# Kernel tuning notes

Measured on AMD Instinct MI355X. Metric: run time of the kernel, lower is better.

## Reference

```python
import jax, jax.numpy as jnp
import numpy as np

B = 4; C = 3; IMG = 256; P = 16; HP = 16; HW = 256
DIM = 512; DEPTH = 6; HEADS = 8; DH = 64
NS = 50; SH = 4; SDH = 64; ITERS = 3; RPD = 128; FF = 2048; N = NS + HW


def _ln(x, g, b):
    m = jnp.mean(x, -1, keepdims=True)
    v = jnp.var(x, -1, keepdims=True)
    return (x - m) * jax.lax.rsqrt(v + 1e-5) * g + b


def _rms(x, g):
    # lucidrains RMSNorm: F.normalize(x, dim=-1) * sqrt(dim) * gamma
    n = jnp.linalg.norm(x, axis=-1, keepdims=True)
    return x / jnp.maximum(n, 1e-12) * (DIM ** 0.5) * g


def setup_inputs() -> dict:
    key = jax.random.key(0)
    ks = iter(jax.random.split(key, 64))
    def W(*s):
        return jax.random.normal(next(ks), s, jnp.float32) * 0.02
    SI = SH * SDH
    d = {}
    d['images'] = jax.random.normal(next(ks), (B, C, IMG, IMG), jnp.float32)
    d['slot_noise'] = jax.random.normal(next(ks), (B, NS, DIM), jnp.float32)
    d['patch_w'] = W(C * P * P, DIM); d['patch_b'] = jnp.zeros((DIM,))
    d['hpos'] = W(HP, DIM); d['wpos'] = W(HP, DIM)
    d['rp_w1'] = W(2, RPD); d['rp_b1'] = jnp.zeros((RPD,))
    d['rp_w2'] = W(RPD, RPD); d['rp_b2'] = jnp.zeros((RPD,))
    d['rp_w3'] = W(RPD, HEADS); d['rp_b3'] = jnp.zeros((HEADS,))
    d['slots_mu'] = W(1, 1, DIM); d['slots_logsigma'] = jnp.zeros((1, 1, DIM))
    d['sa_ln_in_g'] = jnp.ones((DIM,)); d['sa_ln_in_b'] = jnp.zeros((DIM,))
    d['sa_ln_sl_g'] = jnp.ones((DIM,)); d['sa_ln_sl_b'] = jnp.zeros((DIM,))
    d['sa_wq'] = W(DIM, SI); d['sa_bq'] = jnp.zeros((SI,))
    d['sa_wk'] = W(DIM, SI); d['sa_bk'] = jnp.zeros((SI,))
    d['sa_wv'] = W(DIM, SI); d['sa_bv'] = jnp.zeros((SI,))
    d['sa_wo'] = W(SI, DIM); d['sa_bo'] = jnp.zeros((DIM,))
    d['gru_wih'] = W(DIM, 3 * DIM); d['gru_whh'] = W(DIM, 3 * DIM)
    d['gru_bih'] = jnp.zeros((3 * DIM,)); d['gru_bhh'] = jnp.zeros((3 * DIM,))
    d['sa_ln_ff_g'] = jnp.ones((DIM,)); d['sa_ln_ff_b'] = jnp.zeros((DIM,))
    d['sa_mlp_w1'] = W(DIM, DIM); d['sa_mlp_b1'] = jnp.zeros((DIM,))
    d['sa_mlp_w2'] = W(DIM, DIM); d['sa_mlp_b2'] = jnp.zeros((DIM,))
    d['s2c_w'] = W(DIM, 2); d['s2c_b'] = jnp.zeros((2,))
    d['attn_g'] = jnp.ones((DEPTH, DIM))
    d['wq'] = W(DEPTH, DIM, HEADS * DH); d['wk'] = W(DEPTH, DIM, HEADS * DH)
    d['wv'] = W(DEPTH, DIM, HEADS * DH); d['wo'] = W(DEPTH, HEADS * DH, DIM)
    d['ff_g'] = jnp.ones((DEPTH, DIM))
    d['ff_w1'] = W(DEPTH, DIM, FF); d['ff_b1'] = jnp.zeros((DEPTH, FF))
    d['ff_w2'] = W(DEPTH, FF, DIM); d['ff_b2'] = jnp.zeros((DEPTH, DIM))
    d['final_g'] = jnp.ones((DIM,))
    d['pred_w'] = W(DIM, DIM); d['pred_b'] = jnp.zeros((DIM,))
    return d


def reference(images, slot_noise, patch_w, patch_b, hpos, wpos,
              rp_w1, rp_b1, rp_w2, rp_b2, rp_w3, rp_b3,
              slots_mu, slots_logsigma, sa_ln_in_g, sa_ln_in_b, sa_ln_sl_g, sa_ln_sl_b,
              sa_wq, sa_bq, sa_wk, sa_bk, sa_wv, sa_bv, sa_wo, sa_bo,
              gru_wih, gru_whh, gru_bih, gru_bhh, sa_ln_ff_g, sa_ln_ff_b,
              sa_mlp_w1, sa_mlp_b1, sa_mlp_w2, sa_mlp_b2, s2c_w, s2c_b,
              attn_g, wq, wk, wv, wo, ff_g, ff_w1, ff_b1, ff_w2, ff_b2,
              final_g, pred_w, pred_b):
    b = images.shape[0]
    # patchify: b c (h p1) (w p2) -> b h w (p1 p2 c)
    x = images.reshape(b, C, HP, P, HP, P).transpose(0, 2, 4, 3, 5, 1).reshape(b, HP, HP, P * P * C)
    tokens = x @ patch_w + patch_b                     # [b, HP, HP, DIM]
    tokens = tokens + hpos[:, None, :] + wpos[None, :, :]
    tokens = tokens.reshape(b, HW, DIM)
    # --- multi-head slot attention ---
    inp = _ln(tokens, sa_ln_in_g, sa_ln_in_b)
    k = (inp @ sa_wk + sa_bk).reshape(b, HW, SH, SDH).transpose(0, 2, 1, 3)
    v = (inp @ sa_wv + sa_bv).reshape(b, HW, SH, SDH).transpose(0, 2, 1, 3)
    slots = slots_mu + jnp.exp(slots_logsigma) * slot_noise  # [b, NS, DIM]
    scale = SDH ** -0.5
    for _ in range(ITERS):
        prev = slots
        s = _ln(slots, sa_ln_sl_g, sa_ln_sl_b)
        q = (s @ sa_wq + sa_bq).reshape(b, NS, SH, SDH).transpose(0, 2, 1, 3)
        dots = jnp.einsum('bhid,bhjd->bhij', q, k) * scale     # [b, SH, NS, HW]
        attn = jax.nn.softmax(dots, axis=-2) + 1e-8            # softmax over slots
        attn = attn / jnp.sum(attn, -1, keepdims=True)         # weighted mean over inputs
        upd = jnp.einsum('bhij,bhjd->bhid', attn, v)
        upd = upd.transpose(0, 2, 1, 3).reshape(b, NS, SH * SDH) @ sa_wo + sa_bo
        # GRUCell(updates, prev_slots)
        gx = upd @ gru_wih + gru_bih
        gh = prev @ gru_whh + gru_bhh
        xr, xz, xn = jnp.split(gx, 3, -1)
        hr, hz, hn = jnp.split(gh, 3, -1)
        r = jax.nn.sigmoid(xr + hr)
        z = jax.nn.sigmoid(xz + hz)
        nn_ = jnp.tanh(xn + r * hn)
        slots = (1 - z) * nn_ + z * prev
        slots = slots + (jax.nn.relu(_ln(slots, sa_ln_ff_g, sa_ln_ff_b) @ sa_mlp_w1 + sa_mlp_b1) @ sa_mlp_w2 + sa_mlp_b2)
    objects = slots
    slot_coords = objects @ s2c_w + s2c_b              # [b, NS, 2]
    # --- relative position MLP bias (slots coords + patch grid) ---
    g = jnp.arange(HP, dtype=jnp.float32)
    grid = jnp.stack(jnp.meshgrid(g, g, indexing='ij'), -1).reshape(HW, 2)
    coords = jnp.concatenate([slot_coords, jnp.broadcast_to(grid, (b, HW, 2))], axis=1)  # [b, N, 2]
    rel = coords[:, :, None, :] - coords[:, None, :, :]   # [b, N, N, 2]
    hmid = jax.nn.silu(rel @ rp_w1 + rp_b1)
    hmid = jax.nn.silu(hmid @ rp_w2 + rp_b2)
    bias = jnp.transpose(hmid @ rp_w3 + rp_b3, (0, 3, 1, 2))  # [b, HEADS, N, N]
    # --- transformer with per-layer rel-pos bias ---
    x = jnp.concatenate([objects, tokens], axis=1)     # [b, N, DIM]
    ascale = DH ** -0.5
    for l in range(DEPTH):
        h = _rms(x, attn_g[l])
        qh = (h @ wq[l]).reshape(b, N, HEADS, DH).transpose(0, 2, 1, 3)
        kh = (h @ wk[l]).reshape(b, N, HEADS, DH).transpose(0, 2, 1, 3)
        vh = (h @ wv[l]).reshape(b, N, HEADS, DH).transpose(0, 2, 1, 3)
        sim = jnp.einsum('bhid,bhjd->bhij', qh, kh) * ascale + bias
        a = jax.nn.softmax(sim, -1)
        o = jnp.einsum('bhij,bhjd->bhid', a, vh).transpose(0, 2, 1, 3).reshape(b, N, HEADS * DH) @ wo[l]
        x = x + o
        h = _rms(x, ff_g[l])
        x = x + (jax.nn.gelu(h @ ff_w1[l] + ff_b1[l]) @ ff_w2[l] + ff_b2[l])
    x = _rms(x, final_g)
    return x[:, NS:] @ pred_w + pred_b                 # [b, HW, DIM]
```

## Files before the change

kernel.cpp:

```cpp
#include <hip/hip_runtime.h>
#include <hip/hip_bf16.h>

typedef __hip_bfloat16 bf16;
typedef short short8v __attribute__((ext_vector_type(8)));
typedef float float4v __attribute__((ext_vector_type(4)));

static __device__ __forceinline__ float b2f(bf16 x){ return __bfloat162float(x); }

static __device__ __forceinline__ float ldin(const void* p, size_t i, bool isbf) {
  return isbf ? b2f(((const bf16*)p)[i]) : ((const float*)p)[i];
}

static __device__ __forceinline__ unsigned short f2bu(float f) {
  bf16 h = __float2bfloat16(f);
  return *reinterpret_cast<unsigned short*>(&h);
}

#define CDIV(a,b) (((a)+(b)-1)/(b))

#define NB   4
#define NSL  50
#define HWT  256
#define NT   306
#define DIM  512
#define NH   8
#define FF   2048
#define RPP  28100
#define PCH  56200

static __device__ __forceinline__ void rp_decode(int q, int& i, int& j) {
  if (q < 15300) { i = q / NT; j = q % NT; }
  else { int r = q - 15300; i = NSL + r / NSL; j = r % NSL; }
}

__global__ void detect_k(const void* p, int* flag) {
  const unsigned short* u = (const unsigned short*)p;
  int t = threadIdx.x;
  int e = (u[t] >> 7) & 0xFF;
  __shared__ int anybad;
  if (t == 0) anybad = 0;
  __syncthreads();
  if (e >= 0x88) atomicOr(&anybad, 1);
  __syncthreads();
  if (t == 0) *flag = anybad ? 0 : 1;
}

__global__ __launch_bounds__(256) void wtrans_k(const void* __restrict__ W,
    unsigned short* __restrict__ WT, int K, int N, const int* __restrict__ flagp) {
  const bool isbf = *flagp != 0;
  __shared__ unsigned short S[64 * 72];
  const size_t slice = (size_t)K * N * blockIdx.z;
  int n0 = blockIdx.x * 64, k0 = blockIdx.y * 64;
  int t = threadIdx.x;
  int kk = t >> 4, nn = (t & 15) * 4;
#pragma unroll
  for (int r = 0; r < 4; ++r) {
    int k = k0 + kk + r * 16;
    unsigned short v[4];
    if (isbf) {
      ushort4 u = *(const ushort4*)((const unsigned short*)W + slice + (size_t)k * N + n0 + nn);
      v[0]=u.x; v[1]=u.y; v[2]=u.z; v[3]=u.w;
    } else {
      float4 f = *(const float4*)((const float*)W + slice + (size_t)k * N + n0 + nn);
      v[0]=f2bu(f.x); v[1]=f2bu(f.y); v[2]=f2bu(f.z); v[3]=f2bu(f.w);
    }
#pragma unroll
    for (int i = 0; i < 4; ++i) S[(nn + i) * 72 + kk + r * 16] = v[i];
  }
  __syncthreads();
  int nr = t >> 2, kc = (t & 3) * 16;
  short8v s0 = *(const short8v*)&S[nr * 72 + kc];
  short8v s1 = *(const short8v*)&S[nr * 72 + kc + 8];
  unsigned short* dst = WT + slice + (size_t)(n0 + nr) * K + k0 + kc;
  *(short8v*)dst = s0;
  *(short8v*)(dst + 8) = s1;
}

#define LDT 40
static __device__ __forceinline__ void gemm_body2(
    const void* __restrict__ A, int aty,
    const unsigned short* __restrict__ WT,
    const void* __restrict__ bias, size_t boff,
    void* __restrict__ C, int oty,
    int M, int N, int K, int kbeg, int kend,
    int act, int mode, bool isbf)
{
  __shared__ unsigned short As[64 * LDT];
  __shared__ unsigned short Bs[64 * LDT];
  const int tid = threadIdx.x;
  const int lane = tid & 63, wave = tid >> 6;
  const int quad = lane >> 4, ti = lane & 15;
  const int wm = (wave & 1) * 32, wn = (wave >> 1) * 32;
  const int bm = blockIdx.y * 64, bn = blockIdx.x * 64;
  const int srow = tid >> 2, sch = (tid & 3) * 8;

  unsigned short ha[8], hb[8];
  const int gm = bm + srow;
  const bool aok = gm < M;
  const unsigned short* Abf = (const unsigned short*)A + (size_t)gm * K;
  const float*          Af  = (const float*)A + (size_t)gm * K;
  const unsigned short* Bp  = WT + (size_t)(bn + srow) * K;

  auto fetchA = [&](int k0) {
    if (aok) {
      if (aty) {
        const ushort4* ap = (const ushort4*)(Abf + k0 + sch);
        ushort4 u0 = ap[0], u1 = ap[1];
        ha[0]=u0.x; ha[1]=u0.y; ha[2]=u0.z; ha[3]=u0.w;
        ha[4]=u1.x; ha[5]=u1.y; ha[6]=u1.z; ha[7]=u1.w;
      } else {
        const float* ap = Af + k0 + sch;
        float4 x = *(const float4*)ap, y = *(const float4*)(ap + 4);
        ha[0]=f2bu(x.x); ha[1]=f2bu(x.y); ha[2]=f2bu(x.z); ha[3]=f2bu(x.w);
        ha[4]=f2bu(y.x); ha[5]=f2bu(y.y); ha[6]=f2bu(y.z); ha[7]=f2bu(y.w);
      }
    } else {
      for (int i = 0; i < 8; ++i) ha[i] = 0;
    }
  };
  auto fetchB = [&](int k0) {
    const ushort4* bp = (const ushort4*)(Bp + k0 + sch);
    ushort4 u0 = bp[0], u1 = bp[1];
    hb[0]=u0.x; hb[1]=u0.y; hb[2]=u0.z; hb[3]=u0.w;
    hb[4]=u1.x; hb[5]=u1.y; hb[6]=u1.z; hb[7]=u1.w;
  };

  float4v acc00 = {0,0,0,0}, acc01 = {0,0,0,0}, acc10 = {0,0,0,0}, acc11 = {0,0,0,0};
  fetchA(kbeg); fetchB(kbeg);
  for (int k0 = kbeg; k0 < kend; k0 += 32) {
    *(short8v*)&As[srow * LDT + sch] = *(short8v*)ha;
    *(short8v*)&Bs[srow * LDT + sch] = *(short8v*)hb;
    __syncthreads();
    if (k0 + 32 < kend) { fetchA(k0 + 32); fetchB(k0 + 32); }
    short8v a0 = *reinterpret_cast<const short8v*>(&As[(wm + ti)      * LDT + quad * 8]);
    short8v a1 = *reinterpret_cast<const short8v*>(&As[(wm + 16 + ti) * LDT + quad * 8]);
    short8v b0 = *reinterpret_cast<const short8v*>(&Bs[(wn + ti)      * LDT + quad * 8]);
    short8v b1 = *reinterpret_cast<const short8v*>(&Bs[(wn + 16 + ti) * LDT + quad * 8]);
    acc00 = __builtin_amdgcn_mfma_f32_16x16x32_bf16(a0, b0, acc00, 0, 0, 0);
    acc01 = __builtin_amdgcn_mfma_f32_16x16x32_bf16(a0, b1, acc01, 0, 0, 0);
    acc10 = __builtin_amdgcn_mfma_f32_16x16x32_bf16(a1, b0, acc10, 0, 0, 0);
    acc11 = __builtin_amdgcn_mfma_f32_16x16x32_bf16(a1, b1, acc11, 0, 0, 0);
    __syncthreads();
  }

  float4v accs[2][2] = {{acc00, acc01}, {acc10, acc11}};
#pragma unroll
  for (int mi = 0; mi < 2; ++mi) {
#pragma unroll
    for (int ni = 0; ni < 2; ++ni) {
      int row0 = bm + wm + mi * 16 + quad * 4;
      int col  = bn + wn + ni * 16 + ti;
      float bv = (bias && kbeg == 0) ? ldin(bias, boff + col, isbf) : 0.f;
#pragma unroll
      for (int r = 0; r < 4; ++r) {
        int row = row0 + r;
        if (row >= M) continue;
        float v = accs[mi][ni][r] + bv;
        if (act == 1) v = fmaxf(v, 0.f);
        else if (act == 2) {
          float u = 0.7978845608028654f * (v + 0.044715f * v * v * v);
          v = 0.5f * v * (1.f + tanhf(u));
        } else if (act == 3) {
          v = v / (1.f + expf(-v));
        }
        size_t idx = (size_t)row * N + col;
        if (oty) ((bf16*)C)[idx] = __float2bfloat16(v);
        else {
          float* Cf = (float*)C;
          if (mode == 2) atomicAdd(&Cf[idx], v);
          else if (mode == 1) Cf[idx] += v;
          else Cf[idx] = v;
        }
      }
    }
  }
}

__global__ __launch_bounds__(256) void gemm_mfma(
    const void* A, int aty, const unsigned short* WT, size_t woff,
    const void* bias, size_t boff, void* C, int oty,
    int M, int N, int K, int act, int accum, int zsplit, const int* __restrict__ flagp)
{
  int ksz = K / zsplit;
  int kbeg = blockIdx.z * ksz;
  int mode = zsplit > 1 ? 2 : (accum ? 1 : 0);
  gemm_body2(A, aty, WT + woff, bias, boff, C, oty, M, N, K, kbeg, kbeg + ksz,
             act, mode, *flagp != 0);
}

__global__ __launch_bounds__(256) void gemm_mfma_tri(
    const void* A, int aty, const unsigned short* WT, size_t o0, size_t o1, size_t o2,
    void* C0, void* C1, void* C2, int oty, int M, int N, int K,
    const int* __restrict__ flagp)
{
  size_t o = blockIdx.z == 0 ? o0 : (blockIdx.z == 1 ? o1 : o2);
  void* C = blockIdx.z == 0 ? C0 : (blockIdx.z == 1 ? C1 : C2);
  gemm_body2(A, aty, WT + o, nullptr, 0, C, oty, M, N, K, 0, K, 0, 0, *flagp != 0);
}

__global__ __launch_bounds__(256) void gemm_mfma_duo(
    const void* A0, const void* A1, int aty, const unsigned short* WT, size_t o0, size_t o1,
    const void* bias0, const void* bias1, void* C0, void* C1, int oty,
    int M, int N, int K, const int* __restrict__ flagp)
{
  const void* A = blockIdx.z ? A1 : A0;
  size_t o = blockIdx.z ? o1 : o0;
  const void* bias = blockIdx.z ? bias1 : bias0;
  void* C = blockIdx.z ? C1 : C0;
  gemm_body2(A, aty, WT + o, bias, 0, C, oty, M, N, K, 0, K, 0, 0, *flagp != 0);
}

__global__ void s2c_k(const float* __restrict__ slots, const void* __restrict__ w,
                      const void* __restrict__ bv, float* __restrict__ sc,
                      const int* __restrict__ flagp) {
  const bool isbf = *flagp != 0;
  int row = blockIdx.x, t = threadIdx.x;
  const float* x = slots + (size_t)row * DIM;
  float v0 = x[t], v1 = x[t + 256];
  float a0 = v0 * ldin(w, 2 * t, isbf)     + v1 * ldin(w, 2 * (t + 256), isbf);
  float a1 = v0 * ldin(w, 2 * t + 1, isbf) + v1 * ldin(w, 2 * (t + 256) + 1, isbf);
  __shared__ float r0[256], r1[256];
  r0[t] = a0; r1[t] = a1;
  __syncthreads();
  for (int o = 128; o > 0; o >>= 1) {
    if (t < o) { r0[t] += r0[t + o]; r1[t] += r1[t + o]; }
    __syncthreads();
  }
  if (t == 0) {
    sc[row * 2]     = r0[0] + ldin(bv, 0, isbf);
    sc[row * 2 + 1] = r1[0] + ldin(bv, 1, isbf);
  }
}

__global__ void patchify_k(const void* __restrict__ img, unsigned short* __restrict__ xp,
                           const int* __restrict__ flagp) {
  const bool isbf = *flagp != 0;
  int i = blockIdx.x * 256 + threadIdx.x;
  if (i >= NB * HWT * 768) return;
  int col = i % 768, row = i / 768;
  int c = col % 3, p2 = (col / 3) & 15, p1 = col / 48;
  int w = row & 15, h = (row >> 4) & 15, b = row >> 8;
  xp[i] = f2bu(ldin(img, (((size_t)(b * 3 + c) * 256 + h * 16 + p1) * 256) + w * 16 + p2, isbf));
}

__global__ void addpos_k(float* __restrict__ tok, const void* __restrict__ hp,
                         const void* __restrict__ wp, const int* __restrict__ flagp) {
  const bool isbf = *flagp != 0;
  int i = blockIdx.x * 256 + threadIdx.x;
  if (i >= NB * HWT * DIM) return;
  int d = i & 511;
  int row = i >> 9;
  int w = row & 15, h = (row >> 4) & 15;
  tok[i] += ldin(hp, h * DIM + d, isbf) + ldin(wp, w * DIM + d, isbf);
}

__global__ void ln512_k(const float* __restrict__ X, const void* __restrict__ g,
                        const void* __restrict__ b, unsigned short* __restrict__ Y,
                        const int* __restrict__ flagp) {
  const bool isbf = *flagp != 0;
  int row = blockIdx.x, t = threadIdx.x;
  const float* x = X + (size_t)row * DIM;
  float v0 = x[t], v1 = x[t + 256];
  __shared__ float rs[256], rq[256];
  rs[t] = v0 + v1; rq[t] = v0 * v0 + v1 * v1;
  __syncthreads();
  for (int o = 128; o > 0; o >>= 1) {
    if (t < o) { rs[t] += rs[t + o]; rq[t] += rq[t + o]; }
    __syncthreads();
  }
  float mean = rs[0] * (1.f / 512.f);
  float var  = rq[0] * (1.f / 512.f) - mean * mean;
  float inv  = rsqrtf(var + 1e-5f);
  unsigned short* y = Y + (size_t)row * DIM;
  y[t]       = f2bu((v0 - mean) * inv * ldin(g, t, isbf)       + ldin(b, t, isbf));
  y[t + 256] = f2bu((v1 - mean) * inv * ldin(g, t + 256, isbf) + ldin(b, t + 256, isbf));
}

__global__ void rms512_k(const float* __restrict__ X, const void* __restrict__ g,
                         int goff, unsigned short* __restrict__ Y, const int* __restrict__ flagp) {
  const bool isbf = *flagp != 0;
  int row = blockIdx.x, t = threadIdx.x;
  const float* x = X + (size_t)row * DIM;
  float v0 = x[t], v1 = x[t + 256];
  __shared__ float rq[256];
  rq[t] = v0 * v0 + v1 * v1;
  __syncthreads();
  for (int o = 128; o > 0; o >>= 1) {
    if (t < o) rq[t] += rq[t + o];
    __syncthreads();
  }
  float nrm = sqrtf(rq[0]);
  float sc = 22.62741699796952f / fmaxf(nrm, 1e-12f);
  unsigned short* y = Y + (size_t)row * DIM;
  y[t]       = f2bu(v0 * sc * ldin(g, goff + t, isbf));
  y[t + 256] = f2bu(v1 * sc * ldin(g, goff + t + 256, isbf));
}

__global__ void slots_init_k(const void* __restrict__ mu, const void* __restrict__ ls,
                             const void* __restrict__ noise, float* __restrict__ slots,
                             const int* __restrict__ flagp) {
  const bool isbf = *flagp != 0;
  int i = blockIdx.x * 256 + threadIdx.x;
  if (i >= NB * NSL * DIM) return;
  int d = i & 511;
  slots[i] = ldin(mu, d, isbf) + expf(ldin(ls, d, isbf)) * ldin(noise, i, isbf);
}

__global__ void slot_dots_k(const float* __restrict__ q, const float* __restrict__ k,
                            float* __restrict__ dots) {
  int blk = blockIdx.x;
  int i = blk % 50, h = (blk / 50) & 3, b = blk / 200;
  int j = threadIdx.x;
  __shared__ float qs[64];
  if (threadIdx.x < 64) qs[threadIdx.x] = q[((size_t)(b * 50 + i)) * 256 + h * 64 + threadIdx.x];
  __syncthreads();
  const float* kr = k + ((size_t)(b * 256 + j)) * 256 + h * 64;
  float s = 0.f;
#pragma unroll 8
  for (int d = 0; d < 64; ++d) s = fmaf(qs[d], kr[d], s);
  dots[(((size_t)(b * 4 + h) * 50) + i) * 256 + j] = s * 0.125f;
}

__global__ void softmax_slots_k(float* __restrict__ dots) {
  int idx = blockIdx.x * 256 + threadIdx.x;
  if (idx >= 4096) return;
  int j = idx & 255, h = (idx >> 8) & 3, b = idx >> 10;
  float* base = dots + ((size_t)(b * 4 + h) * 50) * 256 + j;
  float m = -1e30f;
  for (int i = 0; i < 50; ++i) m = fmaxf(m, base[i * 256]);
  float s = 0.f;
  for (int i = 0; i < 50; ++i) { float e = expf(base[i * 256] - m); base[i * 256] = e; s += e; }
  float inv = 1.f / s;
  for (int i = 0; i < 50; ++i) base[i * 256] *= inv;
}

__global__ void renorm_attn_k(float* __restrict__ attn) {
  int t = threadIdx.x;
  float* row = attn + (size_t)blockIdx.x * 256;
  float v = row[t] + 1e-8f;
  __shared__ float rs[256];
  rs[t] = v;
  __syncthreads();
  for (int o = 128; o > 0; o >>= 1) {
    if (t < o) rs[t] += rs[t + o];
    __syncthreads();
  }
  row[t] = v / rs[0];
}

__global__ void slot_upd_k(const float* __restrict__ attn, const float* __restrict__ v,
                           float* __restrict__ upd) {
  int bi = blockIdx.x;
  int b = bi / 50, i = bi % 50;
  int t = threadIdx.x, h = t >> 6;
  const float* arow = attn + ((size_t)((b * 4 + h) * 50) + i) * 256;
  float s = 0.f;
  for (int j = 0; j < 256; ++j) s = fmaf(arow[j], v[((size_t)(b * 256 + j)) * 256 + t], s);
  upd[(size_t)bi * 256 + t] = s;
}

__global__ void gru_k(const float* __restrict__ gx, const float* __restrict__ gh,
                      float* __restrict__ slots) {
  int i = blockIdx.x * 256 + threadIdx.x;
  if (i >= NB * NSL * DIM) return;
  int row = i >> 9, d = i & 511;
  size_t b3 = (size_t)row * 1536;
  float xr = gx[b3 + d], xz = gx[b3 + 512 + d], xn = gx[b3 + 1024 + d];
  float hr = gh[b3 + d], hz = gh[b3 + 512 + d], hn = gh[b3 + 1024 + d];
  float r = 1.f / (1.f + expf(-(xr + hr)));
  float z = 1.f / (1.f + expf(-(xz + hz)));
  float n = tanhf(xn + r * hn);
  float prev = slots[i];
  slots[i] = (1.f - z) * n + z * prev;
}

__global__ void build_coords_k(const float* __restrict__ sc, float* __restrict__ coords) {
  int i = blockIdx.x * 256 + threadIdx.x;
  if (i >= NB * NT) return;
  int b = i / NT, n = i % NT;
  float cx, cy;
  if (n < NSL) { cx = sc[(b * NSL + n) * 2]; cy = sc[(b * NSL + n) * 2 + 1]; }
  else { int t = n - NSL; cx = (float)(t >> 4); cy = (float)(t & 15); }
  coords[i * 2] = cx; coords[i * 2 + 1] = cy;
}

__global__ void relpos_table_k(const void* w1, const void* b1, const void* w2,
                               const void* b2, const void* w3, const void* b3,
                               float* __restrict__ tab, const int* __restrict__ flagp) {
  const bool isbf = *flagp != 0;
  int blk = blockIdx.x;
  float r0 = (float)(blk / 31 - 15), r1 = (float)(blk % 31 - 15);
  int t = threadIdx.x;
  __shared__ float h1[128], h2[128];
  float a = fmaf(r0, ldin(w1, t, isbf), fmaf(r1, ldin(w1, 128 + t, isbf), ldin(b1, t, isbf)));
  h1[t] = a / (1.f + expf(-a));
  __syncthreads();
  float s = ldin(b2, t, isbf);
#pragma unroll 4
  for (int k = 0; k < 128; ++k) s = fmaf(h1[k], ldin(w2, k * 128 + t, isbf), s);
  h2[t] = s / (1.f + expf(-s));
  __syncthreads();
  if (t < 8) {
    float o = ldin(b3, t, isbf);
#pragma unroll 4
    for (int k = 0; k < 128; ++k) o = fmaf(h2[k], ldin(w3, k * 8 + t, isbf), o);
    tab[blk * 8 + t] = o;
  }
}

__global__ void bias_fill_k(const float* __restrict__ tab, float* __restrict__ bias) {
  int i = blockIdx.x * 256 + threadIdx.x;
  if (i >= NB * NH * HWT * HWT) return;
  int jj = i & 255, ii = (i >> 8) & 255, h = (i >> 16) & 7, b = i >> 19;
  int di = (ii >> 4) - (jj >> 4) + 15;
  int dj = (ii & 15) - (jj & 15) + 15;
  bias[(((size_t)(b * NH + h) * NT) + NSL + ii) * NT + NSL + jj] = tab[(di * 31 + dj) * 8 + h];
}

__global__ void rp_l1_k(const float* __restrict__ coords, const void* w1, const void* b1,
                        unsigned short* __restrict__ H, int pbase, int pcount,
                        const int* __restrict__ flagp) {
  const bool isbf = *flagp != 0;
  int idx = blockIdx.x * 256 + threadIdx.x;
  if (idx >= pcount * 128) return;
  int pl = idx >> 7, u = idx & 127;
  int p = pbase + pl;
  int q = p % RPP, bb = p / RPP;
  int ii, jj;
  rp_decode(q, ii, jj);
  float r0 = coords[(bb * NT + ii) * 2]     - coords[(bb * NT + jj) * 2];
  float r1 = coords[(bb * NT + ii) * 2 + 1] - coords[(bb * NT + jj) * 2 + 1];
  float a = fmaf(r0, ldin(w1, u, isbf), fmaf(r1, ldin(w1, 128 + u, isbf), ldin(b1, u, isbf)));
  H[(size_t)pl * 128 + u] = f2bu(a / (1.f + expf(-a)));
}

__global__ __launch_bounds__(256) void rp_l3_k(
    const unsigned short* __restrict__ H2, const void* w3, const void* b3,
    float* __restrict__ bias, int pbase, int pcount, const int* __restrict__ flagp) {
  const bool isbf = *flagp != 0;
  __shared__ float W3s[128 * 8];
  int t = threadIdx.x;
// ... 159 lines not shown
      if (row_g < NT)
        Ob[((size_t)(b * NT + row_g)) * DIM + h * 64 + dim] = f2bu(oacc[ntl][r]);
    }
  }
}

__global__ void write_out_k(const float* __restrict__ tmp, void* __restrict__ out,
                            const int* __restrict__ flagp) {
  const bool isbf = *flagp != 0;
  int i = blockIdx.x * 256 + threadIdx.x;
  if (i >= NB * HWT * DIM) return;
  int d = i & 511, tt = (i >> 9) & 255, b = i / (HWT * DIM);
  float v = tmp[((size_t)(b * NT + NSL + tt)) * DIM + d];
  if (isbf) ((bf16*)out)[i] = __float2bfloat16(v);
  else      ((float*)out)[i] = v;
}

extern "C" void kernel_launch(void* const* d_in, const int* in_sizes, int n_in,
                              void* d_out, int out_size, void* d_ws, size_t ws_size,
                              hipStream_t stream) {
  const void* images        = d_in[0];
  const void* slot_noise    = d_in[1];
  const void* patch_w       = d_in[2];
  const void* patch_b       = d_in[3];
  const void* hpos          = d_in[4];
  const void* wpos          = d_in[5];
  const void* rp_w1         = d_in[6];
  const void* rp_b1         = d_in[7];
  const void* rp_w2         = d_in[8];
  const void* rp_b2         = d_in[9];
  const void* rp_w3         = d_in[10];
  const void* rp_b3         = d_in[11];
  const void* slots_mu      = d_in[12];
  const void* slots_logsig  = d_in[13];
  const void* sa_ln_in_g    = d_in[14];
  const void* sa_ln_in_b    = d_in[15];
  const void* sa_ln_sl_g    = d_in[16];
  const void* sa_ln_sl_b    = d_in[17];
  const void* sa_wq         = d_in[18];
  const void* sa_bq         = d_in[19];
  const void* sa_wk         = d_in[20];
  const void* sa_bk         = d_in[21];
  const void* sa_wv         = d_in[22];
  const void* sa_bv         = d_in[23];
  const void* sa_wo         = d_in[24];
  const void* sa_bo         = d_in[25];
  const void* gru_wih       = d_in[26];
  const void* gru_whh       = d_in[27];
  const void* gru_bih       = d_in[28];
  const void* gru_bhh       = d_in[29];
  const void* sa_ln_ff_g    = d_in[30];
  const void* sa_ln_ff_b    = d_in[31];
  const void* sa_mlp_w1     = d_in[32];
  const void* sa_mlp_b1     = d_in[33];
  const void* sa_mlp_w2     = d_in[34];
  const void* sa_mlp_b2     = d_in[35];
  const void* s2c_w         = d_in[36];
  const void* s2c_b         = d_in[37];
  const void* attn_g        = d_in[38];
  const void* wq            = d_in[39];
  const void* wk            = d_in[40];
  const void* wv            = d_in[41];
  const void* wo            = d_in[42];
  const void* ff_g          = d_in[43];
  const void* ff_w1         = d_in[44];
  const void* ff_b1         = d_in[45];
  const void* ff_w2         = d_in[46];
  const void* ff_b2         = d_in[47];
  const void* final_g       = d_in[48];
  const void* pred_w        = d_in[49];
  const void* pred_b        = d_in[50];

  float* ws = (float*)d_ws;
  int* FLAG = (int*)ws;
  size_t off = 16;
  auto alloc = [&](size_t n) { float* p = ws + off; off += (n + 15) & ~(size_t)15; return p; };
  float* TOK   = alloc((size_t)NB * HWT * DIM);
  unsigned short* INPB = (unsigned short*)alloc((size_t)NB * HWT * DIM / 2);
  float* KB    = alloc((size_t)NB * HWT * 256);
  float* VB    = alloc((size_t)NB * HWT * 256);
  float* SLOTS = alloc((size_t)NB * NSL * DIM);
  unsigned short* SLNB = (unsigned short*)alloc((size_t)NB * NSL * DIM / 2);
  float* QB    = alloc((size_t)NB * NSL * 256);
  float* ATT   = alloc((size_t)NB * 4 * NSL * HWT);
  float* UPD   = alloc((size_t)NB * NSL * 256);
  float* UPDP  = alloc((size_t)NB * NSL * DIM);
  unsigned short* HIDSB = (unsigned short*)alloc((size_t)NB * NSL * DIM / 2);
  float* SC    = alloc((size_t)NB * NSL * 2);
  float* CRD   = alloc((size_t)NB * NT * 2);
  float* TAB   = alloc((size_t)961 * 8);
  float* BIAS  = alloc((size_t)NB * NH * NT * NT);
  float* X     = alloc((size_t)NB * NT * DIM);
  unsigned short* HBB  = (unsigned short*)alloc((size_t)NB * NT * DIM / 2);
  unsigned short* QHB  = (unsigned short*)alloc((size_t)NB * NT * DIM / 2);
  unsigned short* KHB  = (unsigned short*)alloc((size_t)NB * NT * DIM / 2);
  unsigned short* VHB  = (unsigned short*)alloc((size_t)NB * NT * DIM / 2);
  float* SIM   = alloc((size_t)NB * NH * NT * NT);
  unsigned short* PROBB = (unsigned short*)alloc((size_t)NB * NH * NT * 320 / 2);
  unsigned short* OBB  = (unsigned short*)alloc((size_t)NB * NT * DIM / 2);
  unsigned short* FFHB = (unsigned short*)alloc((size_t)NB * NT * FF / 2);
  float* OUTT  = alloc((size_t)NB * NT * DIM);
  (void)PROBB;
  unsigned short* XPB = (unsigned short*)OUTT;
  float* GX = SIM;
  float* GH = SIM + (size_t)NB * NSL * 1536;
  const size_t oPatch = 0;
  const size_t oKw    = oPatch + (size_t)512 * 768;
  const size_t oVw    = oKw    + (size_t)256 * 512;
  const size_t oQw    = oVw    + (size_t)256 * 512;
  const size_t oWo    = oQw    + (size_t)256 * 512;
  const size_t oGih   = oWo    + (size_t)512 * 256;
  const size_t oGhh   = oGih   + (size_t)1536 * 512;
  const size_t oMlp1  = oGhh   + (size_t)1536 * 512;
  const size_t oMlp2  = oMlp1  + (size_t)512 * 512;
  const size_t oRp2   = oMlp2  + (size_t)512 * 512;
  const size_t oWq    = oRp2   + (size_t)128 * 128;
  const size_t oWk    = oWq    + (size_t)6 * 512 * 512;
  const size_t oWv    = oWk    + (size_t)6 * 512 * 512;
  const size_t oWol   = oWv    + (size_t)6 * 512 * 512;
  const size_t oFf1   = oWol   + (size_t)6 * 512 * 512;
  const size_t oFf2   = oFf1   + (size_t)6 * 512 * 2048;
  const size_t oPred  = oFf2   + (size_t)6 * 2048 * 512;
  const size_t wtTotal = oPred + (size_t)512 * 512;
  unsigned short* WTS = (unsigned short*)alloc((wtTotal + 1) / 2);
  (void)ws_size; (void)in_sizes; (void)n_in; (void)out_size;

#define GEMMM(A_, ATY_, WOFF_, BIAS_, BOFF_, C_, OTY_, M_, N_, K_, ACT_, ACC_, ZS_) \
  gemm_mfma<<<dim3((N_)/64, CDIV((M_),64), (ZS_)), 256, 0, stream>>>( \
      A_, ATY_, WTS, (size_t)(WOFF_), BIAS_, (size_t)(BOFF_), C_, OTY_, M_, N_, K_, ACT_, ACC_, ZS_, FLAG)

  const int MROW = NB * NT;
  const int MS   = NB * NSL;

  detect_k<<<1, 256, 0, stream>>>(images, FLAG);
  wtrans_k<<<dim3(8, 12, 1),  256, 0, stream>>>(patch_w,  WTS + oPatch, 768,  512,  FLAG);
  wtrans_k<<<dim3(4, 8, 1),   256, 0, stream>>>(sa_wk,    WTS + oKw,    512,  256,  FLAG);
  wtrans_k<<<dim3(4, 8, 1),   256, 0, stream>>>(sa_wv,    WTS + oVw,    512,  256,  FLAG);
  wtrans_k<<<dim3(4, 8, 1),   256, 0, stream>>>(sa_wq,    WTS + oQw,    512,  256,  FLAG);
  wtrans_k<<<dim3(8, 4, 1),   256, 0, stream>>>(sa_wo,    WTS + oWo,    256,  512,  FLAG);
  wtrans_k<<<dim3(24, 8, 1),  256, 0, stream>>>(gru_wih,  WTS + oGih,   512,  1536, FLAG);
  wtrans_k<<<dim3(24, 8, 1),  256, 0, stream>>>(gru_whh,  WTS + oGhh,   512,  1536, FLAG);
  wtrans_k<<<dim3(8, 8, 1),   256, 0, stream>>>(sa_mlp_w1, WTS + oMlp1, 512,  512,  FLAG);
  wtrans_k<<<dim3(8, 8, 1),   256, 0, stream>>>(sa_mlp_w2, WTS + oMlp2, 512,  512,  FLAG);
  wtrans_k<<<dim3(2, 2, 1),   256, 0, stream>>>(rp_w2,    WTS + oRp2,   128,  128,  FLAG);
  wtrans_k<<<dim3(8, 8, 6),   256, 0, stream>>>(wq,       WTS + oWq,    512,  512,  FLAG);
  wtrans_k<<<dim3(8, 8, 6),   256, 0, stream>>>(wk,       WTS + oWk,    512,  512,  FLAG);
  wtrans_k<<<dim3(8, 8, 6),   256, 0, stream>>>(wv,       WTS + oWv,    512,  512,  FLAG);
  wtrans_k<<<dim3(8, 8, 6),   256, 0, stream>>>(wo,       WTS + oWol,   512,  512,  FLAG);
  wtrans_k<<<dim3(32, 8, 6),  256, 0, stream>>>(ff_w1,    WTS + oFf1,   512,  2048, FLAG);
  wtrans_k<<<dim3(8, 32, 6),  256, 0, stream>>>(ff_w2,    WTS + oFf2,   2048, 512,  FLAG);
  wtrans_k<<<dim3(8, 8, 1),   256, 0, stream>>>(pred_w,   WTS + oPred,  512,  512,  FLAG);

  patchify_k<<<CDIV(NB*HWT*768, 256), 256, 0, stream>>>(images, XPB, FLAG);
  hipMemsetAsync(TOK, 0, (size_t)NB * HWT * DIM * sizeof(float), stream);
  GEMMM(XPB, 1, oPatch, patch_b, 0, TOK, 0, NB*HWT, DIM, 768, 0, 0, 3);
  addpos_k<<<CDIV(NB*HWT*DIM, 256), 256, 0, stream>>>(TOK, hpos, wpos, FLAG);

  ln512_k<<<NB*HWT, 256, 0, stream>>>(TOK, sa_ln_in_g, sa_ln_in_b, INPB, FLAG);
  gemm_mfma_duo<<<dim3(4, 16, 2), 256, 0, stream>>>(
      INPB, INPB, 1, WTS, oKw, oVw, sa_bk, sa_bv, KB, VB, 0, NB*HWT, 256, DIM, FLAG);
  slots_init_k<<<CDIV(NB*NSL*DIM, 256), 256, 0, stream>>>(slots_mu, slots_logsig, slot_noise, SLOTS, FLAG);

  for (int it = 0; it < 3; ++it) {
    ln512_k<<<MS, 256, 0, stream>>>(SLOTS, sa_ln_sl_g, sa_ln_sl_b, SLNB, FLAG);
    GEMMM(SLNB, 1, oQw, sa_bq, 0, QB, 0, MS, 256, DIM, 0, 0, 1);
    slot_dots_k<<<NB*4*NSL, 256, 0, stream>>>(QB, KB, ATT);
    softmax_slots_k<<<16, 256, 0, stream>>>(ATT);
    renorm_attn_k<<<NB*4*NSL, 256, 0, stream>>>(ATT);
    slot_upd_k<<<MS, 256, 0, stream>>>(ATT, VB, UPD);
    GEMMM(UPD, 0, oWo, sa_bo, 0, UPDP, 0, MS, DIM, 256, 0, 0, 1);
    gemm_mfma_duo<<<dim3(24, 4, 2), 256, 0, stream>>>(
        UPDP, SLOTS, 0, WTS, oGih, oGhh, gru_bih, gru_bhh, GX, GH, 0, MS, 1536, DIM, FLAG);
    gru_k<<<CDIV(NB*NSL*DIM, 256), 256, 0, stream>>>(GX, GH, SLOTS);
    ln512_k<<<MS, 256, 0, stream>>>(SLOTS, sa_ln_ff_g, sa_ln_ff_b, SLNB, FLAG);
    GEMMM(SLNB, 1, oMlp1, sa_mlp_b1, 0, HIDSB, 1, MS, DIM, DIM, 1, 0, 1);
    GEMMM(HIDSB, 1, oMlp2, sa_mlp_b2, 0, SLOTS, 0, MS, DIM, DIM, 0, 1, 1);
  }

  s2c_k<<<MS, 256, 0, stream>>>(SLOTS, s2c_w, s2c_b, SC, FLAG);
  build_coords_k<<<CDIV(NB*NT, 256), 256, 0, stream>>>(SC, CRD);
  relpos_table_k<<<961, 128, 0, stream>>>(rp_w1, rp_b1, rp_w2, rp_b2, rp_w3, rp_b3, TAB, FLAG);
  bias_fill_k<<<CDIV(NB*NH*HWT*HWT, 256), 256, 0, stream>>>(TAB, BIAS);
  {
    unsigned short* H1 = HBB;
    unsigned short* H2 = HBB + (size_t)PCH * 128;
    for (int c = 0; c < 2; ++c) {
      int pb = c * PCH;
      rp_l1_k<<<CDIV(PCH*128, 256), 256, 0, stream>>>(CRD, rp_w1, rp_b1, H1, pb, PCH, FLAG);
      GEMMM(H1, 1, oRp2, rp_b2, 0, H2, 1, PCH, 128, 128, 3, 0, 1);
      rp_l3_k<<<CDIV(PCH,32), 256, 0, stream>>>(H2, rp_w3, rp_b3, BIAS, pb, PCH, FLAG);
    }
  }

  build_x_k<<<CDIV(NB*NT*DIM, 256), 256, 0, stream>>>(SLOTS, TOK, X);
  for (int l = 0; l < 6; ++l) {
    size_t lw = (size_t)l * 512 * 512;
    rms512_k<<<MROW, 256, 0, stream>>>(X, attn_g, l * DIM, HBB, FLAG);
    gemm_mfma_tri<<<dim3(8, 20, 3), 256, 0, stream>>>(
        HBB, 1, WTS, oWq + lw, oWk + lw, oWv + lw, QHB, KHB, VHB, 1, MROW, DIM, DIM, FLAG);
    attn_fused_k<<<dim3(10, NB*NH), 256, 0, stream>>>(QHB, KHB, VHB, BIAS, OBB);
    GEMMM(OBB, 1, oWol + lw, (const void*)nullptr, 0, X, 0, MROW, DIM, DIM, 0, 1, 2);
    rms512_k<<<MROW, 256, 0, stream>>>(X, ff_g, l * DIM, HBB, FLAG);
    GEMMM(HBB, 1, oFf1 + (size_t)l * 512 * 2048, ff_b1, l * FF, FFHB, 1, MROW, FF, DIM, 2, 0, 1);
    GEMMM(FFHB, 1, oFf2 + (size_t)l * 2048 * 512, ff_b2, l * DIM, X, 0, MROW, DIM, FF, 0, 1, 4);
  }

  rms512_k<<<MROW, 256, 0, stream>>>(X, final_g, 0, HBB, FLAG);
  hipMemsetAsync(OUTT, 0, (size_t)NB * NT * DIM * sizeof(float), stream);
  GEMMM(HBB, 1, oPred, pred_b, 0, OUTT, 0, MROW, DIM, DIM, 0, 0, 2);
  write_out_k<<<CDIV(NB*HWT*DIM, 256), 256, 0, stream>>>(OUTT, d_out, FLAG);

#undef GEMMM
}
```

Baseline: 1.310 ms.

## Fuse slot-attention kernels, batch weight transposes, and deepen GEMM k-tile

Merges the 17 weight-transpose launches into a single kernel driven by a per-matrix block table. Replaces the separate slot dot, softmax, renormalisation and update kernels with one fused kernel per batch-head that keeps scores in shared memory. Doubles the GEMM k-step to 64 with a wider LDS stride to halve barrier count. The fused slot kernel launches only 16 blocks, trading launch and global round-trips for low parallelism and heavy register use.

```diff
diff --git a/kernel.cpp b/kernel.cpp
--- a/kernel.cpp
+++ b/kernel.cpp
@@ -45,12 +45,31 @@
   if (t == 0) *flag = anybad ? 0 : 1;
 }
 
-__global__ __launch_bounds__(256) void wtrans_k(const void* __restrict__ W,
-    unsigned short* __restrict__ WT, int K, int N, const int* __restrict__ flagp) {
-  const bool isbf = *flagp != 0;
+struct WtArgs {
+  const void* W[17];
+  unsigned long long wto[17];
+  int K[17], N[17];
+  int base[18];
+};
+
+__global__ __launch_bounds__(256) void wtrans_all_k(WtArgs a, unsigned short* __restrict__ WT,
+                                                    const int* __restrict__ flagp) {
+  const bool isbf = *flagp != 0;
+  int bid = blockIdx.x;
+  int idx = 0;
+#pragma unroll
+  for (int i = 1; i < 17; ++i) if (bid >= a.base[i]) idx = i;
+  int t0 = bid - a.base[idx];
+  const int K = a.K[idx], N = a.N[idx];
+  const int tilesN = N >> 6;
+  const int perLayer = tilesN * (K >> 6);
+  const int layer = t0 / perLayer, rem = t0 % perLayer;
+  const int n0 = (rem % tilesN) * 64, k0 = (rem / tilesN) * 64;
+  const void* W = a.W[idx];
+  unsigned short* dst0 = WT + a.wto[idx];
+  const size_t slice = (size_t)K * N * layer;
+
   __shared__ unsigned short S[64 * 72];
-  const size_t slice = (size_t)K * N * blockIdx.z;
-  int n0 = blockIdx.x * 64, k0 = blockIdx.y * 64;
   int t = threadIdx.x;
   int kk = t >> 4, nn = (t & 15) * 4;
 #pragma unroll
@@ -71,12 +90,12 @@
   int nr = t >> 2, kc = (t & 3) * 16;
   short8v s0 = *(const short8v*)&S[nr * 72 + kc];
   short8v s1 = *(const short8v*)&S[nr * 72 + kc + 8];
-  unsigned short* dst = WT + slice + (size_t)(n0 + nr) * K + k0 + kc;
+  unsigned short* dst = dst0 + slice + (size_t)(n0 + nr) * K + k0 + kc;
   *(short8v*)dst = s0;
   *(short8v*)(dst + 8) = s1;
 }
 
-#define LDT 40
+#define LDK 72
 static __device__ __forceinline__ void gemm_body2(
     const void* __restrict__ A, int aty,
     const unsigned short* __restrict__ WT,
@@ -85,16 +104,16 @@
     int M, int N, int K, int kbeg, int kend,
     int act, int mode, bool isbf)
 {
-  __shared__ unsigned short As[64 * LDT];
-  __shared__ unsigned short Bs[64 * LDT];
+  __shared__ unsigned short As[64 * LDK];
+  __shared__ unsigned short Bs[64 * LDK];
   const int tid = threadIdx.x;
   const int lane = tid & 63, wave = tid >> 6;
   const int quad = lane >> 4, ti = lane & 15;
   const int wm = (wave & 1) * 32, wn = (wave >> 1) * 32;
   const int bm = blockIdx.y * 64, bn = blockIdx.x * 64;
-  const int srow = tid >> 2, sch = (tid & 3) * 8;
-
-  unsigned short ha[8], hb[8];
+  const int srow = tid >> 2, sch = (tid & 3) * 16;
+
+  unsigned short ha[16], hb[16];
   const int gm = bm + srow;
   const bool aok = gm < M;
   const unsigned short* Abf = (const unsigned short*)A + (size_t)gm * K;
@@ -105,41 +124,53 @@
     if (aok) {
       if (aty) {
         const ushort4* ap = (const ushort4*)(Abf + k0 + sch);
-        ushort4 u0 = ap[0], u1 = ap[1];
-        ha[0]=u0.x; ha[1]=u0.y; ha[2]=u0.z; ha[3]=u0.w;
-        ha[4]=u1.x; ha[5]=u1.y; ha[6]=u1.z; ha[7]=u1.w;
+#pragma unroll
+        for (int i = 0; i < 4; ++i) {
+          ushort4 u = ap[i];
+          ha[i*4+0]=u.x; ha[i*4+1]=u.y; ha[i*4+2]=u.z; ha[i*4+3]=u.w;
+        }
       } else {
-        const float* ap = Af + k0 + sch;
-        float4 x = *(const float4*)ap, y = *(const float4*)(ap + 4);
-        ha[0]=f2bu(x.x); ha[1]=f2bu(x.y); ha[2]=f2bu(x.z); ha[3]=f2bu(x.w);
-        ha[4]=f2bu(y.x); ha[5]=f2bu(y.y); ha[6]=f2bu(y.z); ha[7]=f2bu(y.w);
+        const float4* ap = (const float4*)(Af + k0 + sch);
+#pragma unroll
+        for (int i = 0; i < 4; ++i) {
+          float4 f = ap[i];
+          ha[i*4+0]=f2bu(f.x); ha[i*4+1]=f2bu(f.y); ha[i*4+2]=f2bu(f.z); ha[i*4+3]=f2bu(f.w);
+        }
       }
     } else {
-      for (int i = 0; i < 8; ++i) ha[i] = 0;
+#pragma unroll
+      for (int i = 0; i < 16; ++i) ha[i] = 0;
     }
   };
   auto fetchB = [&](int k0) {
     const ushort4* bp = (const ushort4*)(Bp + k0 + sch);
-    ushort4 u0 = bp[0], u1 = bp[1];
-    hb[0]=u0.x; hb[1]=u0.y; hb[2]=u0.z; hb[3]=u0.w;
-    hb[4]=u1.x; hb[5]=u1.y; hb[6]=u1.z; hb[7]=u1.w;
+#pragma unroll
+    for (int i = 0; i < 4; ++i) {
+      ushort4 u = bp[i];
+      hb[i*4+0]=u.x; hb[i*4+1]=u.y; hb[i*4+2]=u.z; hb[i*4+3]=u.w;
+    }
   };
 
   float4v acc00 = {0,0,0,0}, acc01 = {0,0,0,0}, acc10 = {0,0,0,0}, acc11 = {0,0,0,0};
   fetchA(kbeg); fetchB(kbeg);
-  for (int k0 = kbeg; k0 < kend; k0 += 32) {
-    *(short8v*)&As[srow * LDT + sch] = *(short8v*)ha;
-    *(short8v*)&Bs[srow * LDT + sch] = *(short8v*)hb;
-    __syncthreads();
-    if (k0 + 32 < kend) { fetchA(k0 + 32); fetchB(k0 + 32); }
-    short8v a0 = *reinterpret_cast<const short8v*>(&As[(wm + ti)      * LDT + quad * 8]);
-    short8v a1 = *reinterpret_cast<const short8v*>(&As[(wm + 16 + ti) * LDT + quad * 8]);
-    short8v b0 = *reinterpret_cast<const short8v*>(&Bs[(wn + ti)      * LDT + quad * 8]);
-    short8v b1 = *reinterpret_cast<const short8v*>(&Bs[(wn + 16 + ti) * LDT + quad * 8]);
-    acc00 = __builtin_amdgcn_mfma_f32_16x16x32_bf16(a0, b0, acc00, 0, 0, 0);
-    acc01 = __builtin_amdgcn_mfma_f32_16x16x32_bf16(a0, b1, acc01, 0, 0, 0);
-    acc10 = __builtin_amdgcn_mfma_f32_16x16x32_bf16(a1, b0, acc10, 0, 0, 0);
-    acc11 = __builtin_amdgcn_mfma_f32_16x16x32_bf16(a1, b1, acc11, 0, 0, 0);
+  for (int k0 = kbeg; k0 < kend; k0 += 64) {
+    *(short8v*)&As[srow * LDK + sch]     = *(short8v*)ha;
+    *(short8v*)&As[srow * LDK + sch + 8] = *(short8v*)(ha + 8);
+    *(short8v*)&Bs[srow * LDK + sch]     = *(short8v*)hb;
+    *(short8v*)&Bs[srow * LDK + sch + 8] = *(short8v*)(hb + 8);
+    __syncthreads();
+    if (k0 + 64 < kend) { fetchA(k0 + 64); fetchB(k0 + 64); }
+#pragma unroll
+    for (int ks = 0; ks < 2; ++ks) {
+      short8v a0 = *reinterpret_cast<const short8v*>(&As[(wm + ti)      * LDK + ks * 32 + quad * 8]);
+      short8v a1 = *reinterpret_cast<const short8v*>(&As[(wm + 16 + ti) * LDK + ks * 32 + quad * 8]);
+      short8v b0 = *reinterpret_cast<const short8v*>(&Bs[(wn + ti)      * LDK + ks * 32 + quad * 8]);
+      short8v b1 = *reinterpret_cast<const short8v*>(&Bs[(wn + 16 + ti) * LDK + ks * 32 + quad * 8]);
+      acc00 = __builtin_amdgcn_mfma_f32_16x16x32_bf16(a0, b0, acc00, 0, 0, 0);
+      acc01 = __builtin_amdgcn_mfma_f32_16x16x32_bf16(a0, b1, acc01, 0, 0, 0);
+      acc10 = __builtin_amdgcn_mfma_f32_16x16x32_bf16(a1, b0, acc10, 0, 0, 0);
+      acc11 = __builtin_amdgcn_mfma_f32_16x16x32_bf16(a1, b1, acc11, 0, 0, 0);
+    }
     __syncthreads();
   }
 
@@ -306,57 +337,79 @@
   slots[i] = ldin(mu, d, isbf) + expf(ldin(ls, d, isbf)) * ldin(noise, i, isbf);
 }
 
-__global__ void slot_dots_k(const float* __restrict__ q, const float* __restrict__ k,
-                            float* __restrict__ dots) {
-  int blk = blockIdx.x;
-  int i = blk % 50, h = (blk / 50) & 3, b = blk / 200;
-  int j = threadIdx.x;
-  __shared__ float qs[64];
-  if (threadIdx.x < 64) qs[threadIdx.x] = q[((size_t)(b * 50 + i)) * 256 + h * 64 + threadIdx.x];
-  __syncthreads();
-  const float* kr = k + ((size_t)(b * 256 + j)) * 256 + h * 64;
-  float s = 0.f;
-#pragma unroll 8
-  for (int d = 0; d < 64; ++d) s = fmaf(qs[d], kr[d], s);
-  dots[(((size_t)(b * 4 + h) * 50) + i) * 256 + j] = s * 0.125f;
-}
-
-__global__ void softmax_slots_k(float* __restrict__ dots) {
-  int idx = blockIdx.x * 256 + threadIdx.x;
-  if (idx >= 4096) return;
-  int j = idx & 255, h = (idx >> 8) & 3, b = idx >> 10;
-  float* base = dots + ((size_t)(b * 4 + h) * 50) * 256 + j;
-  float m = -1e30f;
-  for (int i = 0; i < 50; ++i) m = fmaxf(m, base[i * 256]);
-  float s = 0.f;
-  for (int i = 0; i < 50; ++i) { float e = expf(base[i * 256] - m); base[i * 256] = e; s += e; }
-  float inv = 1.f / s;
-  for (int i = 0; i < 50; ++i) base[i * 256] *= inv;
-}
-
-__global__ void renorm_attn_k(float* __restrict__ attn) {
-  int t = threadIdx.x;
-  float* row = attn + (size_t)blockIdx.x * 256;
-  float v = row[t] + 1e-8f;
-  __shared__ float rs[256];
-  rs[t] = v;
-  __syncthreads();
-  for (int o = 128; o > 0; o >>= 1) {
-    if (t < o) rs[t] += rs[t + o];
-    __syncthreads();
-  }
-  row[t] = v / rs[0];
-}
-
-__global__ void slot_upd_k(const float* __restrict__ attn, const float* __restrict__ v,
-                           float* __restrict__ upd) {
-  int bi = blockIdx.x;
-  int b = bi / 50, i = bi % 50;
-  int t = threadIdx.x, h = t >> 6;
-  const float* arow = attn + ((size_t)((b * 4 + h) * 50) + i) * 256;
-  float s = 0.f;
-  for (int j = 0; j < 256; ++j) s = fmaf(arow[j], v[((size_t)(b * 256 + j)) * 256 + t], s);
-  upd[(size_t)bi * 256 + t] = s;
+__global__ __launch_bounds__(256) void slot_core_k(
+    const float* __restrict__ QB, const float* __restrict__ KB,
+    const float* __restrict__ VB, float* __restrict__ UPD)
+{
+  const int b = blockIdx.x >> 2, h = blockIdx.x & 3;
+  __shared__ float qs[NSL * 68];
+  __shared__ float S[NSL * 260];
+  __shared__ float rs[NSL];
+  const int t = threadIdx.x;
+
+  for (int e = t; e < NSL * 64; e += 256) {
+    int i = e >> 6, d = e & 63;
+    qs[i * 68 + d] = QB[((size_t)(b * NSL + i)) * 256 + h * 64 + d];
+  }
+  __syncthreads();
+
+  {
+    const float* kr = KB + ((size_t)(b * HWT + t)) * 256 + h * 64;
+    float kv[64];
+#pragma unroll
+    for (int d = 0; d < 64; ++d) kv[d] = kr[d];
+    for (int i = 0; i < NSL; ++i) {
+      float s = 0.f;
+#pragma unroll
+      for (int d = 0; d < 64; ++d) s = fmaf(qs[i * 68 + d], kv[d], s);
+      S[i * 260 + t] = s * 0.125f;
+    }
+  }
+  __syncthreads();
+
+  {
+    float m = -1e30f;
+    for (int i = 0; i < NSL; ++i) m = fmaxf(m, S[i * 260 + t]);
+    float s = 0.f;
+    for (int i = 0; i < NSL; ++i) { float e = __expf(S[i * 260 + t] - m); S[i * 260 + t] = e; s += e; }
+    float inv = 1.f / s;
+    for (int i = 0; i < NSL; ++i) S[i * 260 + t] = S[i * 260 + t] * inv + 1e-8f;
+  }
+  __syncthreads();
+
+  {
+    int lane = t & 63, wv = t >> 6;
+    for (int i = wv; i < NSL; i += 4) {
+      float s = S[i * 260 + lane] + S[i * 260 + lane + 64] +
+                S[i * 260 + lane + 128] + S[i * 260 + lane + 192];
+      s += __shfl_xor(s, 1);  s += __shfl_xor(s, 2);  s += __shfl_xor(s, 4);
+      s += __shfl_xor(s, 8);  s += __shfl_xor(s, 16); s += __shfl_xor(s, 32);
+      if (lane == 0) rs[i] = s;
+    }
+  }
+  __syncthreads();
+
+  {
+    int d = t & 63, g = t >> 6;
+    float acc[13] = {};
+    int cnt = (NSL - g + 3) >> 2;
+    for (int j = 0; j < HWT; ++j) {
+      float v = VB[((size_t)(b * HWT + j)) * 256 + h * 64 + d];
+      int ii = g;
+#pragma unroll
+      for (int c = 0; c < 13; ++c) {
+        if (c < cnt) acc[c] = fmaf(S[ii * 260 + j], v, acc[c]);
+        ii += 4;
+      }
+    }
+    int ii = g;
+#pragma unroll
+    for (int c = 0; c < 13; ++c) {
+      if (c < cnt)
+        UPD[((size_t)(b * NSL + ii)) * 256 + h * 64 + d] = acc[c] / rs[ii];
+      ii += 4;
+    }
+  }
 }
 
 __global__ void gru_k(const float* __restrict__ gx, const float* __restrict__ gh,
@@ -682,7 +735,6 @@
   float* SLOTS = alloc((size_t)NB * NSL * DIM);
   unsigned short* SLNB = (unsigned short*)alloc((size_t)NB * NSL * DIM / 2);
   float* QB    = alloc((size_t)NB * NSL * 256);
-  float* ATT   = alloc((size_t)NB * 4 * NSL * HWT);
   float* UPD   = alloc((size_t)NB * NSL * 256);
   float* UPDP  = alloc((size_t)NB * NSL * DIM);
   unsigned short* HIDSB = (unsigned short*)alloc((size_t)NB * NSL * DIM / 2);
@@ -696,11 +748,9 @@
   unsigned short* KHB  = (unsigned short*)alloc((size_t)NB * NT * DIM / 2);
   unsigned short* VHB  = (unsigned short*)alloc((size_t)NB * NT * DIM / 2);
   float* SIM   = alloc((size_t)NB * NH * NT * NT);
-  unsigned short* PROBB = (unsigned short*)alloc((size_t)NB * NH * NT * 320 / 2);
   unsigned short* OBB  = (unsigned short*)alloc((size_t)NB * NT * DIM / 2);
   unsigned short* FFHB = (unsigned short*)alloc((size_t)NB * NT * FF / 2);
   float* OUTT  = alloc((size_t)NB * NT * DIM);
-  (void)PROBB;
   unsigned short* XPB = (unsigned short*)OUTT;
   float* GX = SIM;
   float* GH = SIM + (size_t)NB * NSL * 1536;
@@ -733,23 +783,24 @@
   const int MS   = NB * NSL;
 
   detect_k<<<1, 256, 0, stream>>>(images, FLAG);
-  wtrans_k<<<dim3(8, 12, 1),  256, 0, stream>>>(patch_w,  WTS + oPatch, 768,  512,  FLAG);
-  wtrans_k<<<dim3(4, 8, 1),   256, 0, stream>>>(sa_wk,    WTS + oKw,    512,  256,  FLAG);
-  wtrans_k<<<dim3(4, 8, 1),   256, 0, stream>>>(sa_wv,    WTS + oVw,    512,  256,  FLAG);
-  wtrans_k<<<dim3(4, 8, 1),   256, 0, stream>>>(sa_wq,    WTS + oQw,    512,  256,  FLAG);
-  wtrans_k<<<dim3(8, 4, 1),   256, 0, stream>>>(sa_wo,    WTS + oWo,    256,  512,  FLAG);
-  wtrans_k<<<dim3(24, 8, 1),  256, 0, stream>>>(gru_wih,  WTS + oGih,   512,  1536, FLAG);
-  wtrans_k<<<dim3(24, 8, 1),  256, 0, stream>>>(gru_whh,  WTS + oGhh,   512,  1536, FLAG);
-  wtrans_k<<<dim3(8, 8, 1),   256, 0, stream>>>(sa_mlp_w1, WTS + oMlp1, 512,  512,  FLAG);
-  wtrans_k<<<dim3(8, 8, 1),   256, 0, stream>>>(sa_mlp_w2, WTS + oMlp2, 512,  512,  FLAG);
-  wtrans_k<<<dim3(2, 2, 1),   256, 0, stream>>>(rp_w2,    WTS + oRp2,   128,  128,  FLAG);
-  wtrans_k<<<dim3(8, 8, 6),   256, 0, stream>>>(wq,       WTS + oWq,    512,  512,  FLAG);
-  wtrans_k<<<dim3(8, 8, 6),   256, 0, stream>>>(wk,       WTS + oWk,    512,  512,  FLAG);
-  wtrans_k<<<dim3(8, 8, 6),   256, 0, stream>>>(wv,       WTS + oWv,    512,  512,  FLAG);
-  wtrans_k<<<dim3(8, 8, 6),   256, 0, stream>>>(wo,       WTS + oWol,   512,  512,  FLAG);
-  wtrans_k<<<dim3(32, 8, 6),  256, 0, stream>>>(ff_w1,    WTS + oFf1,   512,  2048, FLAG);
-  wtrans_k<<<dim3(8, 32, 6),  256, 0, stream>>>(ff_w2,    WTS + oFf2,   2048, 512,  FLAG);
-  wtrans_k<<<dim3(8, 8, 1),   256, 0, stream>>>(pred_w,   WTS + oPred,  512,  512,  FLAG);
+  {
+    WtArgs a;
+    const void* Wp[17] = { patch_w, sa_wk, sa_wv, sa_wq, sa_wo, gru_wih, gru_whh,
+                           sa_mlp_w1, sa_mlp_w2, rp_w2, wq, wk, wv, wo, ff_w1, ff_w2, pred_w };
+    const size_t Oo[17] = { oPatch, oKw, oVw, oQw, oWo, oGih, oGhh,
+                            oMlp1, oMlp2, oRp2, oWq, oWk, oWv, oWol, oFf1, oFf2, oPred };
+    const int Kk[17] = {768,512,512,512,256,512,512,512,512,128,512,512,512,512,512,2048,512};
+    const int Nn[17] = {512,256,256,256,512,1536,1536,512,512,128,512,512,512,512,2048,512,512};
+    const int Ll[17] = {1,1,1,1,1,1,1,1,1,1,6,6,6,6,6,6,1};
+    int acc = 0;
+    for (int i = 0; i < 17; ++i) {
+      a.W[i] = Wp[i]; a.wto[i] = Oo[i]; a.K[i] = Kk[i]; a.N[i] = Nn[i];
+      a.base[i] = acc;
+      acc += Ll[i] * (Kk[i] >> 6) * (Nn[i] >> 6);
+    }
+    a.base[17] = acc;
+    wtrans_all_k<<<acc, 256, 0, stream>>>(a, WTS, FLAG);
+  }
 
   patchify_k<<<CDIV(NB*HWT*768, 256), 256, 0, stream>>>(images, XPB, FLAG);
   hipMemsetAsync(TOK, 0, (size_t)NB * HWT * DIM * sizeof(float), stream);
@@ -764,10 +815,7 @@
   for (int it = 0; it < 3; ++it) {
     ln512_k<<<MS, 256, 0, stream>>>(SLOTS, sa_ln_sl_g, sa_ln_sl_b, SLNB, FLAG);
     GEMMM(SLNB, 1, oQw, sa_bq, 0, QB, 0, MS, 256, DIM, 0, 0, 1);
-    slot_dots_k<<<NB*4*NSL, 256, 0, stream>>>(QB, KB, ATT);
-    softmax_slots_k<<<16, 256, 0, stream>>>(ATT);
-    renorm_attn_k<<<NB*4*NSL, 256, 0, stream>>>(ATT);
-    slot_upd_k<<<MS, 256, 0, stream>>>(ATT, VB, UPD);
+    slot_core_k<<<16, 256, 0, stream>>>(QB, KB, VB, UPD);
     GEMMM(UPD, 0, oWo, sa_bo, 0, UPDP, 0, MS, DIM, 256, 0, 0, 1);
     gemm_mfma_duo<<<dim3(24, 4, 2), 256, 0, stream>>>(
         UPDP, SLOTS, 0, WTS, oGih, oGhh, gru_bih, gru_bhh, GX, GH, 0, MS, 1536, DIM, FLAG);
```

Result: slower. 1.353 ms (+3.3%).
